# Kernel tuning notes

Hardware: AMD Instinct MI355X
Metric: run time of the kernel (lower is better)

## Reference

```python
import jax, jax.numpy as jnp
import numpy as np

B, L, DIM = 4, 2048, 1024
EXPAND, D_STATE, D_CONV = 2, 16, 4
D_INNER = EXPAND * DIM          # 2048
DT_RANK = DIM // 16             # 64
MLP_HID = 4 * DIM


def setup_inputs() -> dict:
    key = jax.random.key(0)
    ks = jax.random.split(key, 20)
    s = 0.02
    inp = {
        "hidden_states": jax.random.normal(ks[0], (B, L, DIM), jnp.float32),
        "cond": jax.random.normal(ks[1], (B, DIM), jnp.float32),
        # norm (LayerNorm with affine)
        "norm_w": jnp.ones((DIM,), jnp.float32),
        "norm_b": jnp.zeros((DIM,), jnp.float32),
        # adaLN: Linear(dim, 6*dim)
        "ada_w": jax.random.normal(ks[2], (6 * DIM, DIM), jnp.float32) * s,
        "ada_b": jnp.zeros((6 * DIM,), jnp.float32),
        # Mamba mixer params
        "in_proj_w": jax.random.normal(ks[3], (2 * D_INNER, DIM), jnp.float32) * s,
        "conv_w": jax.random.normal(ks[4], (D_INNER, 1, D_CONV), jnp.float32) * s,
        "conv_b": jnp.zeros((D_INNER,), jnp.float32),
        "x_proj_w": jax.random.normal(ks[5], (DT_RANK + 2 * D_STATE, D_INNER), jnp.float32) * s,
        "dt_proj_w": jax.random.normal(ks[6], (D_INNER, DT_RANK), jnp.float32) * s,
        "dt_proj_b": jax.random.uniform(ks[7], (D_INNER,), jnp.float32, -4.0, -2.0),
        "A_log": jnp.log(jnp.broadcast_to(jnp.arange(1, D_STATE + 1, dtype=jnp.float32), (D_INNER, D_STATE))),
        "Dp": jnp.ones((D_INNER,), jnp.float32),
        "out_proj_w": jax.random.normal(ks[8], (DIM, D_INNER), jnp.float32) * s,
        # MLP
        "fc1_w": jax.random.normal(ks[9], (MLP_HID, DIM), jnp.float32) * s,
        "fc1_b": jnp.zeros((MLP_HID,), jnp.float32),
        "fc2_w": jax.random.normal(ks[10], (DIM, MLP_HID), jnp.float32) * s,
        "fc2_b": jnp.zeros((DIM,), jnp.float32),
    }
    return inp


def _layernorm(x, w, b, eps):
    mu = jnp.mean(x, axis=-1, keepdims=True)
    var = jnp.mean(jnp.square(x - mu), axis=-1, keepdims=True)
    y = (x - mu) * jax.lax.rsqrt(var + eps)
    return y * w + b if w is not None else y


def _modulate(x, shift, scale):
    # x: [B,L,D]; shift/scale: [B,D]
    return x * (1.0 + scale[:, None, :]) + shift[:, None, :]


def _mamba(x_in, in_proj_w, conv_w, conv_b, x_proj_w, dt_proj_w, dt_proj_b, A_log, Dp, out_proj_w):
    # x_in: [B,L,DIM]
    xz = jnp.einsum("bld,ed->ble", x_in, in_proj_w)        # [B,L,2*Di]
    x, z = jnp.split(xz, 2, axis=-1)                        # each [B,L,Di]
    # causal depthwise conv over L
    x_ncl = jnp.transpose(x, (0, 2, 1))                     # [B,Di,L]
    x_ncl = jax.lax.conv_general_dilated(
        x_ncl, conv_w, window_strides=(1,), padding=[(D_CONV - 1, 0)],
        feature_group_count=D_INNER, dimension_numbers=("NCH", "OIH", "NCH"))
    x = jnp.transpose(x_ncl, (0, 2, 1)) + conv_b            # [B,L,Di]
    x = jax.nn.silu(x)
    x_dbl = jnp.einsum("bld,ed->ble", x, x_proj_w)          # [B,L,dt_rank+2*N]
    dt, Bm, Cm = jnp.split(x_dbl, [DT_RANK, DT_RANK + D_STATE], axis=-1)
    dt = jax.nn.softplus(jnp.einsum("blr,dr->bld", dt, dt_proj_w) + dt_proj_b)  # [B,L,Di]
    A = -jnp.exp(A_log)                                     # [Di,N]

    def step(h, inps):
        dt_t, B_t, C_t, x_t = inps                          # [B,Di],[B,N],[B,N],[B,Di]
        dA = jnp.exp(dt_t[..., None] * A)                   # [B,Di,N]
        dBx = (dt_t * x_t)[..., None] * B_t[:, None, :]     # [B,Di,N]
        h = h * dA + dBx
        y = jnp.einsum("bdn,bn->bd", h, C_t)
        return h, y

    h0 = jnp.zeros((x.shape[0], D_INNER, D_STATE), x.dtype)
    xs = (jnp.transpose(dt, (1, 0, 2)), jnp.transpose(Bm, (1, 0, 2)),
          jnp.transpose(Cm, (1, 0, 2)), jnp.transpose(x, (1, 0, 2)))
    _, ys = jax.lax.scan(step, h0, xs)                      # [L,B,Di]
    y = jnp.transpose(ys, (1, 0, 2)) + x * Dp               # [B,L,Di]
    y = y * jax.nn.silu(z)
    return jnp.einsum("bld,od->blo", y, out_proj_w)         # [B,L,DIM]


def reference(hidden_states, cond, norm_w, norm_b, ada_w, ada_b, in_proj_w, conv_w,
              conv_b, x_proj_w, dt_proj_w, dt_proj_b, A_log, Dp, out_proj_w,
              fc1_w, fc1_b, fc2_w, fc2_b):
    residual = hidden_states                                # residual=None path
    hs = _layernorm(residual, norm_w, norm_b, 1e-5)
    mods = jax.nn.silu(cond) @ ada_w.T + ada_b              # [B,6*DIM]
    shift_msa, scale_msa, gate_msa, shift_mlp, scale_mlp, gate_mlp = jnp.split(mods, 6, axis=1)
    hs = gate_msa[:, None, :] * _mamba(_modulate(hs, shift_msa, scale_msa),
                                       in_proj_w, conv_w, conv_b, x_proj_w,
                                       dt_proj_w, dt_proj_b, A_log, Dp, out_proj_w)
    h2 = _modulate(_layernorm(hs, None, None, 1e-6), shift_mlp, scale_mlp)
    h2 = jax.nn.gelu(h2 @ fc1_w.T + fc1_b, approximate=True) @ fc2_w.T + fc2_b
    hs = hs + gate_mlp[:, None, :] * h2
    return (hs, residual)
```

## Files before the change

kernel.cpp:

```cpp
#include <hip/hip_runtime.h>
#include <hip/hip_bf16.h>


typedef unsigned short ushort_t;
typedef __attribute__((ext_vector_type(8))) short short8;
typedef __attribute__((ext_vector_type(4))) float floatx4;
typedef __attribute__((ext_vector_type(4))) unsigned short ushort4v;

#define DEVI __device__ __forceinline__

DEVI float b2f(ushort_t u) { union { unsigned int i; float f; } v; v.i = ((unsigned int)u) << 16; return v.f; }
DEVI ushort_t f2b(float f) {
    union { float f; unsigned int i; } v; v.f = f;
    unsigned int r = v.i + 0x7fffu + ((v.i >> 16) & 1u);
    return (ushort_t)(r >> 16);
}
DEVI bool is_f32(const void* nw) { return ((const unsigned int*)nw)[0] == 0x3F800000u; }
DEVI float sigmoidf_(float x) { return 1.f / (1.f + __expf(-x)); }
DEVI float siluf_(float x) { return x * sigmoidf_(x); }
DEVI float softplusf_(float x) { return (x > 20.f) ? x : log1pf(__expf(x)); }
DEVI float gelu_tanh_(float x) {
    float c = 0.7978845608028654f * (x + 0.044715f * x * x * x);
    return 0.5f * x * (1.f + tanhf(c));
}
DEVI void async16(ushort_t* lds, const ushort_t* g) {
    __builtin_amdgcn_global_load_lds((const __attribute__((address_space(1))) void*)g,
                                     (__attribute__((address_space(3))) void*)lds,
                                     16, 0, 0);
}

DEVI void remap_tile(int bid, int Mt, int Nt, int& mt, int& nt) {
    const int nwg = Mt * Nt;
    const int cpx = nwg >> 3;
    const int v = (bid & 7) * cpx + (bid >> 3);
    if (((Mt & 7) == 0) && ((Nt & 7) == 0)) {
        const int s = v >> 6, w = v & 63;
        const int smt = s % (Mt >> 3), snt = s / (Mt >> 3);
        mt = smt * 8 + (w >> 3);
        nt = snt * 8 + (w & 7);
    } else {
        mt = v % Mt;
        nt = v / Mt;
    }
}

__global__ __launch_bounds__(256) void convert_all_kernel(
    const void* __restrict__ in_proj, const void* __restrict__ x_proj,
    const void* __restrict__ dt_w, const void* __restrict__ out_proj,
    const void* __restrict__ fc1_w, const void* __restrict__ fc2_w,
    const void* __restrict__ dt_b, const void* __restrict__ fc1_b,
    const void* __restrict__ fc2_b,
    ushort_t* __restrict__ w_in, ushort_t* __restrict__ w_xp,
    ushort_t* __restrict__ w_dt, ushort_t* __restrict__ w_out,
    ushort_t* __restrict__ w_fc1, ushort_t* __restrict__ w_fc2,
    float* __restrict__ dtb_f, float* __restrict__ fc1b_f,
    float* __restrict__ fc2b_f, const void* __restrict__ nw)
{
    const bool f32 = is_f32(nw);
    int b = blockIdx.x;
    const void* src; ushort_t* dst; int n8;
    if (b < 2048)      { src = in_proj;  dst = w_in;  n8 = 524288; }
    else if (b < 2144) { src = x_proj;   dst = w_xp;  n8 = 24576;  b -= 2048; }
    else if (b < 2208) { src = dt_w;     dst = w_dt;  n8 = 16384;  b -= 2144; }
    else if (b < 3232) { src = out_proj; dst = w_out; n8 = 262144; b -= 2208; }
    else if (b < 5280) { src = fc1_w;    dst = w_fc1; n8 = 524288; b -= 3232; }
    else if (b < 7328) { src = fc2_w;    dst = w_fc2; n8 = 524288; b -= 5280; }
    else {
        b -= 7328;
        const void* bs; float* bd; int n;
        if (b < 8)       { bs = dt_b;  bd = dtb_f;  n = 2048; }
        else if (b < 24) { bs = fc1_b; bd = fc1b_f; n = 4096; b -= 8; }
        else             { bs = fc2_b; bd = fc2b_f; n = 1024; b -= 24; }
        int i = b * 256 + threadIdx.x;
        if (i < n) bd[i] = f32 ? ((const float*)bs)[i] : b2f(((const ushort_t*)bs)[i]);
        return;
    }
    int i = b * 256 + threadIdx.x;
    if (i >= n8) return;
    if (f32) {
        const float4* s = (const float4*)src;
        float4 a = s[2 * i], c = s[2 * i + 1];
        short8 o;
        o[0] = (short)f2b(a.x); o[1] = (short)f2b(a.y);
        o[2] = (short)f2b(a.z); o[3] = (short)f2b(a.w);
        o[4] = (short)f2b(c.x); o[5] = (short)f2b(c.y);
        o[6] = (short)f2b(c.z); o[7] = (short)f2b(c.w);
        ((short8*)dst)[i] = o;
    } else {
        ((short8*)dst)[i] = ((const short8*)src)[i];
    }
}

__global__ __launch_bounds__(256) void ada_kernel(
    const void* __restrict__ condv, const void* __restrict__ ada_wv,
    const void* __restrict__ ada_bv, float* __restrict__ mods,
    const void* __restrict__ nw)
{
    __shared__ float sc[4096];
    const int tid = threadIdx.x;
    const bool f32 = is_f32(nw);
    if (f32) {
        const float* cf = (const float*)condv;
        for (int i = tid; i < 4096; i += 256) sc[i] = siluf_(cf[i]);
    } else {
        const ushort_t* cb = (const ushort_t*)condv;
        for (int i = tid; i < 4096; i += 256) sc[i] = siluf_(b2f(cb[i]));
    }
    __syncthreads();
    const int j = blockIdx.x * 256 + tid;
    float bb = f32 ? ((const float*)ada_bv)[j] : b2f(((const ushort_t*)ada_bv)[j]);
    float s0 = bb, s1 = bb, s2 = bb, s3 = bb;
    if (f32) {
        const float4* w4 = ((const float4*)ada_wv) + (size_t)j * 256;
        for (int d4 = 0; d4 < 256; d4++) {
            float4 w = w4[d4];
            float wv[4] = {w.x, w.y, w.z, w.w};
#pragma unroll
            for (int e = 0; e < 4; e++) {
                int d = d4 * 4 + e;
                s0 += sc[d] * wv[e];
                s1 += sc[1024 + d] * wv[e];
                s2 += sc[2048 + d] * wv[e];
                s3 += sc[3072 + d] * wv[e];
            }
        }
    } else {
        const ushort_t* wrow = ((const ushort_t*)ada_wv) + (size_t)j * 1024;
        for (int d = 0; d < 1024; d += 8) {
            short8 w8 = *(const short8*)(wrow + d);
#pragma unroll
            for (int e = 0; e < 8; e++) {
                float wv = b2f(((const ushort_t*)&w8)[e]);
                s0 += sc[d + e] * wv;
                s1 += sc[1024 + d + e] * wv;
                s2 += sc[2048 + d + e] * wv;
                s3 += sc[3072 + d + e] * wv;
            }
        }
    }
    mods[0 * 6144 + j] = s0;
    mods[1 * 6144 + j] = s1;
    mods[2 * 6144 + j] = s2;
    mods[3 * 6144 + j] = s3;
}

__global__ __launch_bounds__(256) void ln1_res_kernel(
    const void* __restrict__ hiddenv, const void* __restrict__ nwv,
    const void* __restrict__ nbv, const float* __restrict__ mods,
    ushort_t* __restrict__ xout, void* __restrict__ dout)
{
    const int t = blockIdx.x, tid = threadIdx.x;
    const int bb = t >> 11;
    const bool f32 = is_f32(nwv);
    float vv[4], s = 0.f, ss = 0.f;
    if (f32) {
        float4 u = ((const float4*)((const float*)hiddenv + (size_t)t * 1024))[tid];
        vv[0] = u.x; vv[1] = u.y; vv[2] = u.z; vv[3] = u.w;
        ((float4*)((float*)dout + 8388608))[(size_t)t * 256 + tid] = u;
    } else {
        ushort4v u = ((const ushort4v*)((const ushort_t*)hiddenv + (size_t)t * 1024))[tid];
#pragma unroll
        for (int j = 0; j < 4; j++) vv[j] = b2f(u[j]);
        ((ushort4v*)((ushort_t*)dout + 8388608))[(size_t)t * 256 + tid] = u;
    }
#pragma unroll
    for (int j = 0; j < 4; j++) { s += vv[j]; ss += vv[j] * vv[j]; }
#pragma unroll
    for (int off = 32; off > 0; off >>= 1) { s += __shfl_down(s, off); ss += __shfl_down(ss, off); }
    __shared__ float red[8];
    const int wave = tid >> 6, lane = tid & 63;
    if (lane == 0) { red[wave] = s; red[4 + wave] = ss; }
    __syncthreads();
    s = red[0] + red[1] + red[2] + red[3];
    ss = red[4] + red[5] + red[6] + red[7];
    const float mu = s * (1.f / 1024.f);
    const float var = ss * (1.f / 1024.f) - mu * mu;
    const float rstd = rsqrtf(var + 1e-5f);
    const float* mrow = mods + (size_t)bb * 6144;
    ushort4v o;
#pragma unroll
    for (int j = 0; j < 4; j++) {
        int d = tid * 4 + j;
        float w = f32 ? ((const float*)nwv)[d] : b2f(((const ushort_t*)nwv)[d]);
        float b = f32 ? ((const float*)nbv)[d] : b2f(((const ushort_t*)nbv)[d]);
        float y = (vv[j] - mu) * rstd * w + b;
        y = y * (1.f + mrow[1024 + d]) + mrow[d];
        o[j] = f2b(y);
    }
    ((ushort4v*)(xout + (size_t)t * 1024))[tid] = o;
}

__global__ __launch_bounds__(256) void ln2_mod_kernel(
    const ushort_t* __restrict__ hs, const float* __restrict__ mods,
    ushort_t* __restrict__ xout)
{
    const int t = blockIdx.x, tid = threadIdx.x;
    const int bb = t >> 11;
    ushort4v u = ((const ushort4v*)(hs + (size_t)t * 1024))[tid];
    float vv[4], s = 0.f, ss = 0.f;
#pragma unroll
    for (int j = 0; j < 4; j++) { vv[j] = b2f(u[j]); s += vv[j]; ss += vv[j] * vv[j]; }
#pragma unroll
    for (int off = 32; off > 0; off >>= 1) { s += __shfl_down(s, off); ss += __shfl_down(ss, off); }
    __shared__ float red[8];
    const int wave = tid >> 6, lane = tid & 63;
    if (lane == 0) { red[wave] = s; red[4 + wave] = ss; }
    __syncthreads();
    s = red[0] + red[1] + red[2] + red[3];
    ss = red[4] + red[5] + red[6] + red[7];
    const float mu = s * (1.f / 1024.f);
    const float var = ss * (1.f / 1024.f) - mu * mu;
    const float rstd = rsqrtf(var + 1e-6f);
    const float* mrow = mods + (size_t)bb * 6144;
    ushort4v o;
#pragma unroll
    for (int j = 0; j < 4; j++) {
        int d = tid * 4 + j;
        float y = (vv[j] - mu) * rstd;
        y = y * (1.f + mrow[4096 + d]) + mrow[3072 + d];
        o[j] = f2b(y);
    }
    ((ushort4v*)(xout + (size_t)t * 1024))[tid] = o;
}

__global__ __launch_bounds__(256) void conv_silu_kernel(
    const ushort_t* __restrict__ xb, const void* __restrict__ cwv,
    const void* __restrict__ cbv, ushort_t* __restrict__ xc,
    const void* __restrict__ nw)
{
    const int t = blockIdx.x;
    const int l = t & 2047;
    const int c0 = threadIdx.x * 8;
    const bool f32 = is_f32(nw);
    float acc[8];
    float wlf[32];
    if (f32) {
        const float* cbf = (const float*)cbv;
#pragma unroll
        for (int j = 0; j < 8; j++) acc[j] = cbf[c0 + j];
        const float4* cw4 = (const float4*)((const float*)cwv + (size_t)c0 * 4);
#pragma unroll
        for (int q = 0; q < 8; q++) {
            float4 w = cw4[q];
            wlf[q * 4 + 0] = w.x; wlf[q * 4 + 1] = w.y;
            wlf[q * 4 + 2] = w.z; wlf[q * 4 + 3] = w.w;
        }
    } else {
        const ushort_t* cbb = (const ushort_t*)cbv;
#pragma unroll
        for (int j = 0; j < 8; j++) acc[j] = b2f(cbb[c0 + j]);
        const ushort_t* cwb = (const ushort_t*)cwv + (size_t)c0 * 4;
#pragma unroll
        for (int q = 0; q < 32; q++) wlf[q] = b2f(cwb[q]);
    }
#pragma unroll
    for (int k = 0; k < 4; k++) {
        int tl = l + k - 3;
        if (tl < 0) continue;
        short8 xv = *(const short8*)(xb + (size_t)(t + k - 3) * 2048 + c0);
#pragma unroll
        for (int j = 0; j < 8; j++)
            acc[j] += b2f(((const ushort_t*)&xv)[j]) * wlf[j * 4 + k];
    }
    short8 o;
#pragma unroll
    for (int j = 0; j < 8; j++) ((ushort_t*)&o)[j] = f2b(siluf_(acc[j]));
    *(short8*)(xc + (size_t)t * 2048 + c0) = o;
}

__global__ __launch_bounds__(256) void scan_phase1(
    const ushort_t* __restrict__ dtb, const ushort_t* __restrict__ xcv,
    const ushort_t* __restrict__ xdbl, const void* __restrict__ A_logv,
    ushort_t* __restrict__ Hloc, ushort_t* __restrict__ Pst,
    const void* __restrict__ nw)
{
    const int blk = blockIdx.x;
    const int dblk = blk & 7;
    const int c = (blk >> 3) & 31;
    const int b = blk >> 8;
    const int d = dblk * 256 + threadIdx.x;
    const bool f32 = is_f32(nw);
    float Av[16];
#pragma unroll
    for (int n = 0; n < 16; n++) {
        float al = f32 ? ((const float*)A_logv)[(size_t)d * 16 + n]
                       : b2f(((const ushort_t*)A_logv)[(size_t)d * 16 + n]);
        Av[n] = -__expf(al);
    }
    float h[16], Pa[16];
#pragma unroll
    for (int n = 0; n < 16; n++) { h[n] = 0.f; Pa[n] = 1.f; }
    const int t0 = c * 64;
    size_t tb = ((size_t)b * 2048 + t0) * 2048 + d;
    float dtv = b2f(dtb[tb]);
    float xv  = b2f(xcv[tb]);
    for (int tt = 0; tt < 64; ++tt) {
        float dtn = b2f(dtb[tb + 2048]);
        float xn  = b2f(xcv[tb + 2048]);
        const ushort_t* bp = xdbl + ((size_t)b * 2048 + t0 + tt) * 96 + 64;
        short8 B8a = *(const short8*)bp;
        short8 B8b = *(const short8*)(bp + 8);
        float dtx = dtv * xv;
#pragma unroll
        for (int n = 0; n < 8; n++) {
            float dA = __expf(dtv * Av[n]);
            h[n] = h[n] * dA + dtx * b2f(((const ushort_t*)&B8a)[n]);
            Pa[n] *= dA;
        }
#pragma unroll
        for (int n = 8; n < 16; n++) {
            float dA = __expf(dtv * Av[n]);
            h[n] = h[n] * dA + dtx * b2f(((const ushort_t*)&B8b)[n - 8]);
            Pa[n] *= dA;
        }
        dtv = dtn; xv = xn; tb += 2048;
    }
    const size_t o = (((size_t)c * 4 + b) * 16) * 2048 + d;
#pragma unroll
    for (int n = 0; n < 16; n++) {
        Hloc[o + (size_t)n * 2048] = f2b(h[n]);
        Pst [o + (size_t)n * 2048] = f2b(Pa[n]);
    }
}

__global__ __launch_bounds__(256) void scan_phase2(
    const ushort_t* __restrict__ Hloc, const ushort_t* __restrict__ Pst,
    float* __restrict__ Hin)
{
    const int gi = blockIdx.x * 256 + threadIdx.x;
    const int d = gi & 2047;
    const int n = (gi >> 11) & 15;
    const int b = gi >> 15;
    float h = 0.f;
    const size_t o0 = ((size_t)b * 16 + n) * 2048 + d;
    for (int c = 0; c < 32; ++c) {
        const size_t o = o0 + (size_t)c * (4 * 16 * 2048);
        Hin[o] = h;
        h = b2f(Hloc[o]) + b2f(Pst[o]) * h;
    }
}

__global__ __launch_bounds__(256) void scan_phase3(
    const ushort_t* __restrict__ dtb, ushort_t* __restrict__ xc,
    const ushort_t* __restrict__ xdbl, const ushort_t* __restrict__ zbuf,
    const void* __restrict__ A_logv, const void* __restrict__ Dpv,
    const float* __restrict__ Hin, const void* __restrict__ nw)
{
    const int blk = blockIdx.x;
    const int dblk = blk & 7;
    const int c = (blk >> 3) & 31;
    const int b = blk >> 8;
    const int d = dblk * 256 + threadIdx.x;
    const bool f32 = is_f32(nw);
    float Av[16];
#pragma unroll
    for (int n = 0; n < 16; n++) {
        float al = f32 ? ((const float*)A_logv)[(size_t)d * 16 + n]
                       : b2f(((const ushort_t*)A_logv)[(size_t)d * 16 + n]);
        Av[n] = -__expf(al);
    }
    const float Dv = f32 ? ((const float*)Dpv)[d] : b2f(((const ushort_t*)Dpv)[d]);
    float h[16];
    {
        const size_t o = (((size_t)c * 4 + b) * 16) * 2048 + d;
#pragma unroll
        for (int n = 0; n < 16; n++) h[n] = Hin[o + (size_t)n * 2048];
    }
    const int t0 = c * 64;
    size_t tb = ((size_t)b * 2048 + t0) * 2048 + d;
    float dtv = b2f(dtb[tb]);
    float xv  = b2f(xc[tb]);
    float zv  = b2f(zbuf[tb]);
    for (int tt = 0; tt < 64; ++tt) {
        float dtn = b2f(dtb[tb + 2048]);
        float xn  = b2f(xc[tb + 2048]);
        float zn  = b2f(zbuf[tb + 2048]);
        const ushort_t* bp = xdbl + ((size_t)b * 2048 + t0 + tt) * 96 + 64;
        short8 B8a = *(const short8*)bp;
        short8 B8b = *(const short8*)(bp + 8);
        short8 C8a = *(const short8*)(bp + 16);
        short8 C8b = *(const short8*)(bp + 24);
        float dtx = dtv * xv;
        float y = 0.f;
#pragma unroll
        for (int n = 0; n < 8; n++) {
            float dA = __expf(dtv * Av[n]);
            h[n] = h[n] * dA + dtx * b2f(((const ushort_t*)&B8a)[n]);
            y += h[n] * b2f(((const ushort_t*)&C8a)[n]);
        }
#pragma unroll
        for (int n = 8; n < 16; n++) {
            float dA = __expf(dtv * Av[n]);
            h[n] = h[n] * dA + dtx * b2f(((const ushort_t*)&B8b)[n - 8]);
            y += h[n] * b2f(((const ushort_t*)&C8b)[n - 8]);
        }
        float yo = (y + xv * Dv) * siluf_(zv);
        xc[tb] = f2b(yo);
        dtv = dtn; xv = xn; zv = zn; tb += 2048;
    }
}

template <int EPI>
DEVI void epi_store(int row, int col, float v,
                    void* C0, void* C1, int ldc,
                    const float* bias, const float* mods,
                    const ushort_t* hs, int fl)
{
    if constexpr (EPI == 0) {
        if (col < 2048)
            ((ushort_t*)C0)[(size_t)row * 2048 + col] = f2b(v);
        else
            ((ushort_t*)C1)[(size_t)row * 2048 + (col - 2048)] = f2b(v);
    } else if constexpr (EPI == 1) {
        ((ushort_t*)C0)[(size_t)row * ldc + col] = f2b(v);
    } else if constexpr (EPI == 2) {
        v += bias[col];
        ((ushort_t*)C0)[(size_t)row * ldc + col] = f2b(softplusf_(v));
    } else if constexpr (EPI == 3) {
        const int bb = row >> 11;
        v *= mods[(size_t)bb * 6144 + 2048 + col];
        ((ushort_t*)C0)[(size_t)row * ldc + col] = f2b(v);
    } else if constexpr (EPI == 4) {
        v += bias[col];
        ((ushort_t*)C0)[(size_t)row * ldc + col] = f2b(gelu_tanh_(v));
    } else if constexpr (EPI == 5) {
        v += bias[col];
        const int bb = row >> 11;
        float o = b2f(hs[(size_t)row * 1024 + col]) + mods[(size_t)bb * 6144 + 5120 + col] * v;
        if (fl)
            ((float*)C0)[(size_t)row * ldc + col] = o;
        else
            ((ushort_t*)C0)[(size_t)row * ldc + col] = f2b(o);
    } else if constexpr (EPI == 6) {
        ((float*)C0)[(size_t)row * ldc + col] = v;
    }
}

#define KLOOP_PIPE(NT)                                               \
    stage(0, 0);                                                     \
    {                                                                \
        int cur = 0;                                                 \
        for (int kt = 0; kt < (NT); kt++) {                          \
            if (kt + 1 < (NT)) {                                     \
                stage(cur ^ 1, kt + 1);                              \
                asm volatile("s_waitcnt vmcnt(8)" ::: "memory");     \
            } else {                                                 \
                asm volatile("s_waitcnt vmcnt(0)" ::: "memory");     \
            }                                                        \
            __builtin_amdgcn_sched_barrier(0);                       \
            __builtin_amdgcn_s_barrier();                            \
            __builtin_amdgcn_sched_barrier(0);                       \
            __builtin_amdgcn_s_setprio(1);                           \
            compute(cur);                                            \
            __builtin_amdgcn_s_setprio(0);                           \
            __builtin_amdgcn_sched_barrier(0);                       \
            __builtin_amdgcn_s_barrier();                            \
            __builtin_amdgcn_sched_barrier(0);                       \
            cur ^= 1;                                                \
        }                                                            \
    }

template <int EPI>
__global__ __launch_bounds__(256) void gemm_bt(
    const ushort_t* __restrict__ A, int lda,
    const ushort_t* __restrict__ W, int ldw,
    int M, int N, int K,
    void* __restrict__ C0, void* __restrict__ C1, int ldc,
    const float* __restrict__ bias,
    const float* __restrict__ mods,
    const ushort_t* __restrict__ hs,
    const void* __restrict__ nwp)
{
    __shared__ __align__(16) ushort_t sA[2][128 * 64];
    __shared__ __align__(16) ushort_t sB[2][128 * 64];
    const int tid = threadIdx.x;
    const int wave = tid >> 6, lane = tid & 63;
    int mt, nt;
    if constexpr (EPI == 6) {
        mt = blockIdx.x & 63; nt = 0;
        const int kc = blockIdx.x >> 6;
        A += (size_t)kc * 512;
        W += (size_t)kc * 512;
        C0 = (float*)C0 + (size_t)kc * 8192 * 96;
    } else {
        remap_tile(blockIdx.x, M >> 7, (N + 127) >> 7, mt, nt);
    }
    const int m0 = mt << 7, n0 = nt << 7;
    const int wr = wave >> 1, wc = wave & 1;
    const int r = tid >> 3, c8 = tid & 7;
    const int rs7 = r & 7;
    int fl = 0;
    if constexpr (EPI == 5) fl = is_f32(nwp) ? 1 : 0;

    floatx4 acc[4][4];
#pragma unroll
    for (int m = 0; m < 4; m++)
#pragma unroll
        for (int nn = 0; nn < 4; nn++) acc[m][nn] = floatx4{0.f, 0.f, 0.f, 0.f};

    auto stage = [&](int buf, int kt) {
        const int kb = kt << 6;
#pragma unroll
        for (int i = 0; i < 4; i++) {
            const int row = i * 32 + r;
            async16(&sA[buf][(size_t)row * 64 + c8 * 8],
                    A + (size_t)(m0 + row) * lda + kb + ((c8 ^ rs7) << 3));
            int rB = n0 + row; if (rB >= N) rB = N - 1;
            async16(&sB[buf][(size_t)row * 64 + c8 * 8],
                    W + (size_t)rB * ldw + kb + ((c8 ^ rs7) << 3));
        }
    };
    auto compute = [&](int buf) {
#pragma unroll
        for (int kk = 0; kk < 2; kk++) {
            const int sw = ((kk * 4 + (lane >> 4)) ^ (lane & 7)) << 3;
            short8 bfr[4];
#pragma unroll
            for (int nn = 0; nn < 4; nn++)
                bfr[nn] = *(const short8*)&sB[buf][(size_t)(wc * 64 + nn * 16 + (lane & 15)) * 64 + sw];
#pragma unroll
            for (int m = 0; m < 4; m++) {
                short8 af = *(const short8*)&sA[buf][(size_t)(wr * 64 + m * 16 + (lane & 15)) * 64 + sw];
#pragma unroll
                for (int nn = 0; nn < 4; nn++)
                    acc[m][nn] = __builtin_amdgcn_mfma_f32_16x16x32_bf16(af, bfr[nn], acc[m][nn], 0, 0, 0);
            }
        }
    };

    const int NT = K >> 6;
    KLOOP_PIPE(NT)

    const int erow = wr * 64 + ((lane >> 4) << 2);
    const int ecol = wc * 64 + (lane & 15);
#pragma unroll
    for (int m = 0; m < 4; m++)
#pragma unroll
        for (int nn = 0; nn < 4; nn++) {
            const int col = n0 + ecol + nn * 16;
            if (col >= N) continue;
#pragma unroll
            for (int rr = 0; rr < 4; rr++)
                epi_store<EPI>(m0 + erow + m * 16 + rr, col, acc[m][nn][rr],
                               C0, C1, ldc, bias, mods, hs, fl);
        }
}

template <int EPI>
__global__ __launch_bounds__(512) void gemm256(
    const ushort_t* __restrict__ A, int lda,
    const ushort_t* __restrict__ W, int ldw,
    int M, int N, int K,
    void* __restrict__ C0, void* __restrict__ C1, int ldc,
    const float* __restrict__ bias,
    const float* __restrict__ mods,
    const ushort_t* __restrict__ hs,
    const void* __restrict__ nwp)
{
    __shared__ __align__(16) ushort_t sA[2][4][256 * 16];
    __shared__ __align__(16) ushort_t sB[2][4][256 * 16];
    const int tid = threadIdx.x;
    const int wave = tid >> 6, lane = tid & 63;
    const int l15 = lane & 15, j8 = lane >> 4;
    int mt, nt;
    remap_tile(blockIdx.x, M >> 8, N >> 8, mt, nt);
    const int m0 = mt << 8, n0 = nt << 8;
    const int wr = wave >> 2, wc = wave & 3;
    const int srow = tid >> 1, scs = tid & 1;
    const int ssrc = scs ^ ((srow >> 2) & 1);
    int fl = 0;
    if constexpr (EPI == 5) fl = is_f32(nwp) ? 1 : 0;

    floatx4 acc[8][4];
#pragma unroll
    for (int m = 0; m < 8; m++)
#pragma unroll
        for (int nn = 0; nn < 4; nn++) acc[m][nn] = floatx4{0.f, 0.f, 0.f, 0.f};

    auto stage = [&](int buf, int kt, int p) {
        const int kb = (kt << 6) + (p << 4);
        async16(&sA[buf][p][srow * 16 + scs * 8],
                A + (size_t)(m0 + srow) * lda + kb + ssrc * 8);
        async16(&sB[buf][p][srow * 16 + scs * 8],
                W + (size_t)(n0 + srow) * ldw + kb + ssrc * 8);
    };

#define G256_PHASE(P, MLO, KK)                                                  \
    {                                                                           \
        if (pre) {                                                              \
            stage(cur ^ 1, kt + 1, P);                                          \
            asm volatile("s_waitcnt vmcnt(4)" ::: "memory");                    \
        } else if (P == 2) {                                                    \
            asm volatile("s_waitcnt vmcnt(0)" ::: "memory");                    \
        }                                                                       \
        __builtin_amdgcn_sched_barrier(0);                                      \
        __builtin_amdgcn_s_barrier();                                           \
        __builtin_amdgcn_sched_barrier(0);                                      \
        short8 bfr[4], af[4];                                                   \
        _Pragma("unroll")                                                       \
        for (int nn = 0; nn < 4; nn++) {                                        \
            const int row = wc * 64 + nn * 16 + l15;                            \
            bfr[nn] = *(const short8*)&sB[cur][(KK) * 2 + (j8 >> 1)]            \
                          [row * 16 + (((j8 & 1) ^ ((row >> 2) & 1)) << 3)];    \
        }                                                                       \
        _Pragma("unroll")                                                       \
        for (int i = 0; i < 4; i++) {                                           \
            const int row = wr * 128 + ((MLO) + i) * 16 + l15;                  \
            af[i] = *(const short8*)&sA[cur][(KK) * 2 + (j8 >> 1)]              \
                        [row * 16 + (((j8 & 1) ^ ((row >> 2) & 1)) << 3)];      \
        }                                                                       \
        __builtin_amdgcn_s_setprio(1);                                          \
        _Pragma("unroll")                                                       \
        for (int i = 0; i < 4; i++)                                             \
            _Pragma("unroll")                                                   \
            for (int nn = 0; nn < 4; nn++)                                      \
                acc[(MLO) + i][nn] = __builtin_amdgcn_mfma_f32_16x16x32_bf16(   \
                    af[i], bfr[nn], acc[(MLO) + i][nn], 0, 0, 0);               \
        __builtin_amdgcn_s_setprio(0);                                          \
    }

    const int NT = K >> 6;
#pragma unroll
    for (int p = 0; p < 4; p++) stage(0, 0, p);
    int cur = 0;
    for (int kt = 0; kt < NT; kt++) {
        const bool pre = (kt + 1 < NT);
        G256_PHASE(0, 0, 0)
        G256_PHASE(1, 4, 0)
        G256_PHASE(2, 0, 1)
        G256_PHASE(3, 4, 1)
        __builtin_amdgcn_sched_barrier(0);
        __builtin_amdgcn_s_barrier();
        __builtin_amdgcn_sched_barrier(0);
        cur ^= 1;
    }
#undef G256_PHASE

    const int erow = wr * 128 + (j8 << 2);
    const int ecol = wc * 64 + l15;
#pragma unroll
    for (int m = 0; m < 8; m++)
#pragma unroll
        for (int nn = 0; nn < 4; nn++) {
            const int col = n0 + ecol + nn * 16;
            if (col >= N) continue;
#pragma unroll
            for (int rr = 0; rr < 4; rr++)
                epi_store<EPI>(m0 + erow + m * 16 + rr, col, acc[m][nn][rr],
                               C0, C1, ldc, bias, mods, hs, fl);
        }
}

__global__ __launch_bounds__(256) void xp_reduce_kernel(
    const float* __restrict__ part, ushort_t* __restrict__ x_dbl)
{
    const int i = blockIdx.x * 256 + threadIdx.x;
    float s = part[i] + part[i + 786432] + part[i + 2 * 786432] + part[i + 3 * 786432];
    x_dbl[i] = f2b(s);
}

extern "C" void kernel_launch(void* const* d_in, const int* in_sizes, int n_in,
                              void* d_out, int out_size, void* d_ws, size_t ws_size,
                              hipStream_t stream)
{
    const void* hidden   = d_in[0];
    const void* cond     = d_in[1];
    const void* norm_w   = d_in[2];
    const void* norm_b   = d_in[3];
    const void* ada_w    = d_in[4];
    const void* ada_b    = d_in[5];
    const void* in_proj  = d_in[6];
    const void* conv_w   = d_in[7];
    const void* conv_b   = d_in[8];
    const void* x_proj   = d_in[9];
    const void* dt_w     = d_in[10];
    const void* dt_b     = d_in[11];
    const void* A_log    = d_in[12];
    const void* Dp       = d_in[13];
    const void* out_proj = d_in[14];
    const void* fc1_w    = d_in[15];
    const void* fc1_b    = d_in[16];
    const void* fc2_w    = d_in[17];
    const void* fc2_b    = d_in[18];

    constexpr size_t OFF_MODS  = 256;
    constexpr size_t OFF_DTB_F = 131072;
    constexpr size_t OFF_FC1B  = 139264;
    constexpr size_t OFF_FC2B  = 155648;
    constexpr size_t OFF_WIN   = 262144;
    constexpr size_t OFF_WXP   = 8650752;
    constexpr size_t OFF_WDT   = 9043968;
    constexpr size_t OFF_WOUT  = 9306112;
    constexpr size_t OFF_WFC1  = 13500416;
    constexpr size_t OFF_WFC2  = 21889024;
    constexpr size_t OFF_XBUF  = 30277632;
    constexpr size_t OFF_ZBUF  = 63832064;
    constexpr size_t OFF_XCONV = 97386496;
    constexpr size_t OFF_XIN   = 130940928;
    constexpr size_t OFF_XDBL  = 147718144;
    constexpr size_t OFF_HS    = 149291008;
    constexpr size_t WS_NEED   = 166068224;
    if (ws_size < WS_NEED) return;

    char* ws = (char*)d_ws;
    float*    mods   = (float*)(ws + OFF_MODS);
    float*    dtb_f  = (float*)(ws + OFF_DTB_F);
    float*    fc1b_f = (float*)(ws + OFF_FC1B);
    float*    fc2b_f = (float*)(ws + OFF_FC2B);
    ushort_t* w_in   = (ushort_t*)(ws + OFF_WIN);
    ushort_t* w_xp   = (ushort_t*)(ws + OFF_WXP);
    ushort_t* w_dt   = (ushort_t*)(ws + OFF_WDT);
    ushort_t* w_out  = (ushort_t*)(ws + OFF_WOUT);
    ushort_t* w_fc1  = (ushort_t*)(ws + OFF_WFC1);
    ushort_t* w_fc2  = (ushort_t*)(ws + OFF_WFC2);
    ushort_t* xbuf   = (ushort_t*)(ws + OFF_XBUF);
    ushort_t* zbuf   = (ushort_t*)(ws + OFF_ZBUF);
    ushort_t* x_conv = (ushort_t*)(ws + OFF_XCONV);
    ushort_t* x_in   = (ushort_t*)(ws + OFF_XIN);
    ushort_t* x_dbl  = (ushort_t*)(ws + OFF_XDBL);
    ushort_t* hsb    = (ushort_t*)(ws + OFF_HS);
    ushort_t* dtb    = xbuf;
    ushort_t* h1     = xbuf;
    ushort_t* h2in   = x_in;
    float*    xp_part= (float*)(ws + OFF_XIN);
    ushort_t* Hloc   = (ushort_t*)(ws + OFF_XIN);
    ushort_t* Pst    = (ushort_t*)(ws + OFF_XIN + 8388608);
    float*    Hin    = (float*)(ws + OFF_HS);

    convert_all_kernel<<<7356, 256, 0, stream>>>(
        in_proj, x_proj, dt_w, out_proj, fc1_w, fc2_w, dt_b, fc1_b, fc2_b,
        w_in, w_xp, w_dt, w_out, w_fc1, w_fc2, dtb_f, fc1b_f, fc2b_f, norm_w);

    ada_kernel<<<24, 256, 0, stream>>>(cond, ada_w, ada_b, mods, norm_w);
    ln1_res_kernel<<<8192, 256, 0, stream>>>(hidden, norm_w, norm_b, mods, x_in, d_out);
    gemm256<0><<<512, 512, 0, stream>>>(x_in, 1024, w_in, 1024, 8192, 4096, 1024,
                                        xbuf, zbuf, 2048, nullptr, nullptr, nullptr, nullptr);
    conv_silu_kernel<<<8192, 256, 0, stream>>>(xbuf, conv_w, conv_b, x_conv, norm_w);
    gemm_bt<6><<<256, 256, 0, stream>>>(x_conv, 2048, w_xp, 2048, 8192, 96, 512,
                                        xp_part, nullptr, 96, nullptr, nullptr, nullptr, nullptr);
    xp_reduce_kernel<<<3072, 256, 0, stream>>>(xp_part, x_dbl);
    gemm_bt<2><<<1024, 256, 0, stream>>>(x_dbl, 96, w_dt, 64, 8192, 2048, 64,
                                         dtb, nullptr, 2048, dtb_f, nullptr, nullptr, nullptr);
    scan_phase1<<<1024, 256, 0, stream>>>(dtb, x_conv, x_dbl, A_log, Hloc, Pst, norm_w);
    scan_phase2<<<512, 256, 0, stream>>>(Hloc, Pst, Hin);
    scan_phase3<<<1024, 256, 0, stream>>>(dtb, x_conv, x_dbl, zbuf, A_log, Dp, Hin, norm_w);
    gemm_bt<3><<<512, 256, 0, stream>>>(x_conv, 2048, w_out, 2048, 8192, 1024, 2048,
                                        hsb, nullptr, 1024, nullptr, mods, nullptr, nullptr);
    ln2_mod_kernel<<<8192, 256, 0, stream>>>(hsb, mods, h2in);
    gemm256<4><<<512, 512, 0, stream>>>(h2in, 1024, w_fc1, 1024, 8192, 4096, 1024,
                                        h1, nullptr, 4096, fc1b_f, nullptr, nullptr, nullptr);
    gemm_bt<5><<<512, 256, 0, stream>>>(h1, 4096, w_fc2, 4096, 8192, 1024, 4096,
                                        d_out, nullptr, 1024, fc2b_f, mods, hsb, norm_w);
}
```

Measured before the change: 757.0 us.

## Double-buffer LDS fragment reads in 256-tile GEMM to overlap with MFMA

Restructures the GEMM main loop so the LDS fragment reads for the next phase are issued before the MFMAs of the current phase, using two register fragment sets (A/B ping-pong). The first fragment of the next k-tile is prefetched at the end of each iteration, and the vmcnt waits are rearranged around the new order. The aim is to hide LDS read latency behind matrix-core work. In exchange it uses more VGPRs and adds subtle barrier and wait-count ordering that must stay correct.

```diff
diff --git a/kernel.cpp b/kernel.cpp
--- a/kernel.cpp
+++ b/kernel.cpp
@@ -585,56 +585,78 @@
                 W + (size_t)(n0 + srow) * ldw + kb + ssrc * 8);
     };
 
-#define G256_PHASE(P, MLO, KK)                                                  \
+    short8 afA[4], bfA[4], afB[4], bfB[4];
+
+#define RD256(AF, BF, BUF, KK, MLO)                                             \
     {                                                                           \
-        if (pre) {                                                              \
-            stage(cur ^ 1, kt + 1, P);                                          \
-            asm volatile("s_waitcnt vmcnt(4)" ::: "memory");                    \
-        } else if (P == 2) {                                                    \
-            asm volatile("s_waitcnt vmcnt(0)" ::: "memory");                    \
-        }                                                                       \
-        __builtin_amdgcn_sched_barrier(0);                                      \
-        __builtin_amdgcn_s_barrier();                                           \
-        __builtin_amdgcn_sched_barrier(0);                                      \
-        short8 bfr[4], af[4];                                                   \
+        const int sl_ = (KK) * 2 + (j8 >> 1);                                   \
+        const int h_ = j8 & 1;                                                  \
         _Pragma("unroll")                                                       \
         for (int nn = 0; nn < 4; nn++) {                                        \
-            const int row = wc * 64 + nn * 16 + l15;                            \
-            bfr[nn] = *(const short8*)&sB[cur][(KK) * 2 + (j8 >> 1)]            \
-                          [row * 16 + (((j8 & 1) ^ ((row >> 2) & 1)) << 3)];    \
+            const int row_ = wc * 64 + nn * 16 + l15;                           \
+            BF[nn] = *(const short8*)&sB[BUF][sl_]                              \
+                         [row_ * 16 + ((h_ ^ ((row_ >> 2) & 1)) << 3)];         \
         }                                                                       \
         _Pragma("unroll")                                                       \
         for (int i = 0; i < 4; i++) {                                           \
-            const int row = wr * 128 + ((MLO) + i) * 16 + l15;                  \
-            af[i] = *(const short8*)&sA[cur][(KK) * 2 + (j8 >> 1)]              \
-                        [row * 16 + (((j8 & 1) ^ ((row >> 2) & 1)) << 3)];      \
+            const int row_ = wr * 128 + ((MLO) + i) * 16 + l15;                 \
+            AF[i] = *(const short8*)&sA[BUF][sl_]                               \
+                        [row_ * 16 + ((h_ ^ ((row_ >> 2) & 1)) << 3)];          \
         }                                                                       \
+    }
+
+#define MM256(AF, BF, MLO)                                                      \
+    {                                                                           \
         __builtin_amdgcn_s_setprio(1);                                          \
         _Pragma("unroll")                                                       \
         for (int i = 0; i < 4; i++)                                             \
             _Pragma("unroll")                                                   \
             for (int nn = 0; nn < 4; nn++)                                      \
                 acc[(MLO) + i][nn] = __builtin_amdgcn_mfma_f32_16x16x32_bf16(   \
-                    af[i], bfr[nn], acc[(MLO) + i][nn], 0, 0, 0);               \
+                    AF[i], BF[nn], acc[(MLO) + i][nn], 0, 0, 0);                \
         __builtin_amdgcn_s_setprio(0);                                          \
     }
 
+#define SBAR256                                                                 \
+    __builtin_amdgcn_sched_barrier(0);                                          \
+    __builtin_amdgcn_s_barrier();                                               \
+    __builtin_amdgcn_sched_barrier(0);
+
     const int NT = K >> 6;
 #pragma unroll
     for (int p = 0; p < 4; p++) stage(0, 0, p);
+    asm volatile("s_waitcnt vmcnt(4)" ::: "memory");
+    SBAR256
+    RD256(afA, bfA, 0, 0, 0)
     int cur = 0;
     for (int kt = 0; kt < NT; kt++) {
         const bool pre = (kt + 1 < NT);
-        G256_PHASE(0, 0, 0)
-        G256_PHASE(1, 4, 0)
-        G256_PHASE(2, 0, 1)
-        G256_PHASE(3, 4, 1)
-        __builtin_amdgcn_sched_barrier(0);
-        __builtin_amdgcn_s_barrier();
-        __builtin_amdgcn_sched_barrier(0);
+        if (pre) stage(cur ^ 1, kt + 1, 0);
+        RD256(afB, bfB, cur, 0, 4)
+        MM256(afA, bfA, 0)
+        if (pre) { asm volatile("s_waitcnt vmcnt(2)" ::: "memory"); }
+        else     { asm volatile("s_waitcnt vmcnt(0)" ::: "memory"); }
+        SBAR256
+        if (pre) stage(cur ^ 1, kt + 1, 1);
+        RD256(afA, bfA, cur, 1, 0)
+        MM256(afB, bfB, 4)
+        SBAR256
+        if (pre) stage(cur ^ 1, kt + 1, 2);
+        RD256(afB, bfB, cur, 1, 4)
+        MM256(afA, bfA, 0)
+        if (pre) { asm volatile("s_waitcnt vmcnt(2)" ::: "memory"); }
+        SBAR256
+        if (pre) {
+            stage(cur ^ 1, kt + 1, 3);
+            RD256(afA, bfA, cur ^ 1, 0, 0)
+        }
+        MM256(afB, bfB, 4)
+        SBAR256
         cur ^= 1;
     }
-#undef G256_PHASE
+#undef RD256
+#undef MM256
+#undef SBAR256
 
     const int erow = wr * 128 + (j8 << 2);
     const int ecol = wc * 64 + l15;
```

New measurement: 766.5 us. No clear change (+1.3%).
